# Kernel optimization log

Measured on AMD Instinct MI355X. Metric: run time of the kernel, lower is better.

Reference implementation:

```python
import jax, jax.numpy as jnp
import numpy as np

N, DIM = 8192, 128

def setup_inputs() -> dict:
    key = jax.random.key(0)
    ks = jax.random.split(key, 9)
    s = 1.0 / np.sqrt(DIM)
    return {
        "x": jax.random.normal(ks[0], (N, DIM), dtype=jnp.float32),
        "Wq": jax.random.uniform(ks[1], (DIM, DIM), jnp.float32, -s, s),
        "bq": jax.random.uniform(ks[2], (DIM,), jnp.float32, -s, s),
        "Wk": jax.random.uniform(ks[3], (DIM, DIM), jnp.float32, -s, s),
        "bk": jax.random.uniform(ks[4], (DIM,), jnp.float32, -s, s),
        "Wv": jax.random.uniform(ks[5], (DIM, DIM), jnp.float32, -s, s),
        "bv": jax.random.uniform(ks[6], (DIM,), jnp.float32, -s, s),
        "Wo": jax.random.uniform(ks[7], (DIM, DIM), jnp.float32, -s, s),
        "bo": jax.random.uniform(ks[8], (DIM,), jnp.float32, -s, s),
    }

def reference(x, Wq, bq, Wk, bk, Wv, bv, Wo, bo):
    # nn.Linear: y = x @ W.T + b
    Q = x @ Wq.T + bq                      # [N, d]
    K = x @ Wk.T + bk                      # [N, d]
    V = x @ Wv.T + bv                      # [N, d]
    scale = 1.0 / jnp.sqrt(jnp.asarray(x.shape[-1], x.dtype))
    scores = (Q @ K.T) * scale             # [N, N] — matches original O(n^2) math
    attn = jax.nn.softmax(scores, axis=-1)
    out = attn @ V                         # [N, d]
    return out @ Wo.T + bo
```

## Files before the change

### kernel.cpp

```cpp
#include <hip/hip_runtime.h>
#include <math.h>


typedef __bf16 bf16x8 __attribute__((ext_vector_type(8)));
typedef float f32x4 __attribute__((ext_vector_type(4)));
typedef float f32x16 __attribute__((ext_vector_type(16)));
typedef unsigned int u32x4 __attribute__((ext_vector_type(4)));
typedef unsigned int u32x2 __attribute__((ext_vector_type(2)));
typedef unsigned short us16;

#define NTOK 8192
#define CHUNKS 8

static constexpr float SCALE_L2E = 0.08838834764831845f * 1.4426950408889634f;

__device__ __forceinline__ unsigned f2bf_u(float x) {
    unsigned u = __builtin_bit_cast(unsigned, x);
    return (u + 0x7FFFu + ((u >> 16) & 1u)) >> 16;
}

__device__ __forceinline__ unsigned pk_bf16(float x, float y) {
    unsigned a = __builtin_bit_cast(unsigned, x) + 0x8000u;
    unsigned b = __builtin_bit_cast(unsigned, y) + 0x8000u;
#if __has_builtin(__builtin_amdgcn_perm)
    return __builtin_amdgcn_perm(b, a, 0x07060302u);
#else
    return (a >> 16) | (b & 0xFFFF0000u);
#endif
}

__device__ __forceinline__ unsigned cvtpk_bf16(float x, float y) {
    unsigned r;
    asm("v_cvt_pk_bf16_f32 %0, %1, %2" : "=v"(r) : "v"(x), "v"(y));
    return r;
}

__device__ __forceinline__ void plswap(unsigned& a, unsigned& b) {
    asm("v_permlane32_swap_b32 %0, %1" : "+v"(a), "+v"(b));
}

__device__ __forceinline__ void pl16swap(unsigned& a, unsigned& b) {
    asm("v_permlane16_swap_b32 %0, %1" : "+v"(a), "+v"(b));
}

__device__ __forceinline__ float fexp2(float x) {
#if __has_builtin(__builtin_amdgcn_exp2f)
    return __builtin_amdgcn_exp2f(x);
#else
    return exp2f(x);
#endif
}

__device__ __forceinline__ bf16x8 ld_frag(const us16* p) {
    u32x4 u = *reinterpret_cast<const u32x4*>(p);
    return __builtin_bit_cast(bf16x8, u);
}

__device__ __forceinline__ bf16x8 cvt_frag(const float* p) {
    f32x4 a = *reinterpret_cast<const f32x4*>(p);
    f32x4 b = *reinterpret_cast<const f32x4*>(p + 4);
    u32x4 o;
    o[0] = f2bf_u(a[0]) | (f2bf_u(a[1]) << 16);
    o[1] = f2bf_u(a[2]) | (f2bf_u(a[3]) << 16);
    o[2] = f2bf_u(b[0]) | (f2bf_u(b[1]) << 16);
    o[3] = f2bf_u(b[2]) | (f2bf_u(b[3]) << 16);
    return __builtin_bit_cast(bf16x8, o);
}

__global__ __launch_bounds__(256) void proj_qkv(
    const float* __restrict__ x,
    const float* __restrict__ wq, const float* __restrict__ bq,
    const float* __restrict__ wk, const float* __restrict__ bk,
    const float* __restrict__ wv, const float* __restrict__ bv,
    us16* __restrict__ Qb, us16* __restrict__ Kb, us16* __restrict__ Vt)
{
    __shared__ us16 ldsT[4][16 * 136];

    int z = blockIdx.x >> 7;
    int tile = blockIdx.x & 127;
    const float* W = z == 0 ? wq : z == 1 ? wk : wv;
    const float* bias = z == 0 ? bq : z == 1 ? bk : bv;
    float osc = z == 0 ? SCALE_L2E : 1.0f;

    int w = threadIdx.x >> 6, lane = threadIdx.x & 63;
    int quad = lane >> 4, l15 = lane & 15;
    int rbase = tile * 64 + w * 16;

    bf16x8 af[4];
#pragma unroll
    for (int ks = 0; ks < 4; ++ks)
        af[ks] = cvt_frag(x + (rbase + l15) * 128 + ks * 32 + quad * 8);

    f32x4 acc[8];
#pragma unroll
    for (int nt = 0; nt < 8; ++nt) acc[nt] = f32x4{0.f, 0.f, 0.f, 0.f};

#pragma unroll
    for (int nt = 0; nt < 8; ++nt) {
#pragma unroll
        for (int ks = 0; ks < 4; ++ks) {
            bf16x8 bf = cvt_frag(W + (nt * 16 + l15) * 128 + ks * 32 + quad * 8);
            acc[nt] = __builtin_amdgcn_mfma_f32_16x16x32_bf16(af[ks], bf, acc[nt], 0, 0, 0);
        }
    }

    if (z < 2) {
        us16* T = &ldsT[w][0];
        us16* Out = z == 0 ? Qb : Kb;
#pragma unroll
        for (int nt = 0; nt < 8; ++nt) {
            float bb = bias[nt * 16 + l15];
#pragma unroll
            for (int r = 0; r < 4; ++r)
                T[(quad * 4 + r) * 136 + nt * 16 + l15] =
                    (us16)f2bf_u((acc[nt][r] + bb) * osc);
        }
        asm volatile("s_waitcnt lgkmcnt(0)" ::: "memory");
        __builtin_amdgcn_sched_barrier(0);
        int row = lane >> 2, seg = lane & 3;
        const us16* src = T + row * 136 + seg * 32;
        us16* dst = Out + (rbase + row) * 128 + seg * 32;
#pragma unroll
        for (int c = 0; c < 4; ++c)
            *reinterpret_cast<u32x4*>(dst + c * 8) =
                *reinterpret_cast<const u32x4*>(src + c * 8);
    } else {
#pragma unroll
        for (int nt = 0; nt < 8; ++nt) {
            float bb = bias[nt * 16 + l15];
            int d = nt * 16 + l15, r0 = rbase + quad * 4;
            u32x2 pk;
            pk[0] = f2bf_u(acc[nt][0] + bb) | (f2bf_u(acc[nt][1] + bb) << 16);
            pk[1] = f2bf_u(acc[nt][2] + bb) | (f2bf_u(acc[nt][3] + bb) << 16);
            *reinterpret_cast<u32x2*>(Vt + d * NTOK + r0) = pk;
        }
    }
}

__global__ __launch_bounds__(256, 2) void attn(
    const us16* __restrict__ Qb, const us16* __restrict__ Kb,
    const us16* __restrict__ Vt,
    float* __restrict__ Opart, float* __restrict__ Lpart)
{
    __shared__ us16 ldsK[64 * 136];
    __shared__ us16 ldsV[128 * 72];

    int qtile = blockIdx.x >> 3, chunk = blockIdx.x & 7;
    int tid = threadIdx.x, w = tid >> 6, lane = tid & 63;
    int quad = lane >> 4, l15 = lane & 15;
    int qb0 = qtile * 128 + w * 32;

    bf16x8 qf[2][4];
#pragma unroll
    for (int mt = 0; mt < 2; ++mt)
#pragma unroll
        for (int ks = 0; ks < 4; ++ks)
            qf[mt][ks] = ld_frag(Qb + (qb0 + mt * 16 + l15) * 128 + ks * 32 + quad * 8);

    f32x4 o[2][8];
#pragma unroll
    for (int mt = 0; mt < 2; ++mt)
#pragma unroll
        for (int dt = 0; dt < 8; ++dt) o[mt][dt] = f32x4{0.f, 0.f, 0.f, 0.f};

    f32x4 lacc[2];
    lacc[0] = f32x4{0.f, 0.f, 0.f, 0.f};
    lacc[1] = f32x4{0.f, 0.f, 0.f, 0.f};

    u32x4 onesu;
    onesu[0] = onesu[1] = onesu[2] = onesu[3] = 0x3F803F80u;
    bf16x8 ones = __builtin_bit_cast(bf16x8, onesu);

    for (int it = 0; it < 16; ++it) {
        int kk = chunk * 1024 + it * 64;
#pragma unroll
        for (int c = 0; c < 4; ++c) {
            int idx = tid + c * 256;
            int r = idx >> 4, cc = idx & 15;
            *reinterpret_cast<u32x4*>(ldsK + r * 136 + cc * 8) =
                *reinterpret_cast<const u32x4*>(Kb + (kk + r) * 128 + cc * 8);
        }
#pragma unroll
        for (int c = 0; c < 4; ++c) {
            int idx = tid + c * 256;
            int r = idx >> 3, cc = idx & 7;
            *reinterpret_cast<u32x4*>(ldsV + r * 72 + cc * 8) =
                *reinterpret_cast<const u32x4*>(Vt + r * NTOK + kk + cc * 8);
        }
        __syncthreads();

        f32x4 s[2][4];
#pragma unroll
        for (int mt = 0; mt < 2; ++mt)
#pragma unroll
            for (int nt = 0; nt < 4; ++nt) s[mt][nt] = f32x4{0.f, 0.f, 0.f, 0.f};

        __builtin_amdgcn_s_setprio(1);
#pragma unroll
        for (int nt = 0; nt < 4; ++nt) {
#pragma unroll
            for (int ks = 0; ks < 4; ++ks) {
                bf16x8 kf = ld_frag(ldsK + (nt * 16 + l15) * 136 + ks * 32 + quad * 8);
                s[0][nt] = __builtin_amdgcn_mfma_f32_16x16x32_bf16(kf, qf[0][ks], s[0][nt], 0, 0, 0);
                s[1][nt] = __builtin_amdgcn_mfma_f32_16x16x32_bf16(kf, qf[1][ks], s[1][nt], 0, 0, 0);
            }
        }
        __builtin_amdgcn_s_setprio(0);

        bf16x8 afP[2][2];
#pragma unroll
        for (int mt = 0; mt < 2; ++mt) {
            unsigned W[4][2];
#pragma unroll
            for (int nt = 0; nt < 4; ++nt) {
                float p0 = fexp2(s[mt][nt][0]);
                float p1 = fexp2(s[mt][nt][1]);
                float p2 = fexp2(s[mt][nt][2]);
                float p3 = fexp2(s[mt][nt][3]);
                W[nt][0] = cvtpk_bf16(p0, p1);
                W[nt][1] = cvtpk_bf16(p2, p3);
            }
#pragma unroll
            for (int k2 = 0; k2 < 2; ++k2) {
                u32x4 f;
                {
                    unsigned X = W[2 * k2][0], Y = W[2 * k2 + 1][0];
                    plswap(X, Y); pl16swap(X, Y);
                    f[0] = X; f[2] = Y;
                }
                {
                    unsigned X = W[2 * k2][1], Y = W[2 * k2 + 1][1];
                    plswap(X, Y); pl16swap(X, Y);
                    f[1] = X; f[3] = Y;
                }
                afP[mt][k2] = __builtin_bit_cast(bf16x8, f);
            }
        }

        lacc[0] = __builtin_amdgcn_mfma_f32_16x16x32_bf16(afP[0][0], ones, lacc[0], 0, 0, 0);
        lacc[0] = __builtin_amdgcn_mfma_f32_16x16x32_bf16(afP[0][1], ones, lacc[0], 0, 0, 0);
        lacc[1] = __builtin_amdgcn_mfma_f32_16x16x32_bf16(afP[1][0], ones, lacc[1], 0, 0, 0);
        lacc[1] = __builtin_amdgcn_mfma_f32_16x16x32_bf16(afP[1][1], ones, lacc[1], 0, 0, 0);

        __builtin_amdgcn_s_setprio(1);
#pragma unroll
        for (int dt = 0; dt < 8; ++dt) {
#pragma unroll
            for (int k2 = 0; k2 < 2; ++k2) {
                bf16x8 bv = ld_frag(ldsV + (dt * 16 + l15) * 72 + k2 * 32 + quad * 8);
                o[0][dt] = __builtin_amdgcn_mfma_f32_16x16x32_bf16(afP[0][k2], bv, o[0][dt], 0, 0, 0);
                o[1][dt] = __builtin_amdgcn_mfma_f32_16x16x32_bf16(afP[1][k2], bv, o[1][dt], 0, 0, 0);
            }
        }
        __builtin_amdgcn_s_setprio(0);
        __syncthreads();
    }

#pragma unroll
    for (int mt = 0; mt < 2; ++mt)
#pragma unroll
        for (int dt = 0; dt < 8; ++dt)
#pragma unroll
            for (int r = 0; r < 4; ++r) {
                int row = qb0 + mt * 16 + quad * 4 + r;
                Opart[(size_t)(chunk * NTOK + row) * 128 + dt * 16 + l15] = o[mt][dt][r];
            }
    if (l15 == 0) {
#pragma unroll
        for (int mt = 0; mt < 2; ++mt)
#pragma unroll
            for (int r = 0; r < 4; ++r) {
                int row = qb0 + mt * 16 + quad * 4 + r;
                Lpart[chunk * NTOK + row] = lacc[mt][r];
            }
    }
}

__global__ __launch_bounds__(256) void combine_proj(
    const float* __restrict__ Opart, const float* __restrict__ Lpart,
    const float* __restrict__ Wo, const float* __restrict__ bo,
    float* __restrict__ out)
{
    __shared__ us16 ldsO[32 * 136];
    __shared__ float ldsL[32];

    int tile = blockIdx.x, t = threadIdx.x;
    int r0 = tile * 32;

    if (t < 32) {
        float L = 0.f;
#pragma unroll
        for (int c = 0; c < CHUNKS; ++c) L += Lpart[c * NTOK + r0 + t];
        ldsL[t] = 1.0f / L;
    }

    f32x4 acc[4];
#pragma unroll
    for (int j = 0; j < 4; ++j) acc[j] = f32x4{0.f, 0.f, 0.f, 0.f};

#pragma unroll
    for (int c = 0; c < CHUNKS; ++c) {
        const float* src = Opart + (size_t)(c * NTOK + r0) * 128;
#pragma unroll
        for (int j = 0; j < 4; ++j) {
            f32x4 v = *reinterpret_cast<const f32x4*>(src + j * 1024 + t * 4);
            acc[j] += v;
        }
    }
    __syncthreads();

#pragma unroll
    for (int j = 0; j < 4; ++j) {
        int flat = j * 1024 + t * 4;
        int row = flat >> 7, col = flat & 127;
        float sc = ldsL[row];
        u32x2 wv;
        wv[0] = pk_bf16(acc[j][0] * sc, acc[j][1] * sc);
        wv[1] = pk_bf16(acc[j][2] * sc, acc[j][3] * sc);
        *reinterpret_cast<u32x2*>(ldsO + row * 136 + col) = wv;
    }
    __syncthreads();

    int w = t >> 6, lane = t & 63;
    int l31 = lane & 31, hi = lane >> 5;

    bf16x8 af[8];
#pragma unroll
    for (int ks = 0; ks < 8; ++ks)
        af[ks] = ld_frag(ldsO + l31 * 136 + ks * 16 + hi * 8);

    f32x16 acc2;
#pragma unroll
    for (int r = 0; r < 16; ++r) acc2[r] = 0.f;

#pragma unroll
    for (int ks = 0; ks < 8; ++ks) {
        bf16x8 bfw = cvt_frag(Wo + (w * 32 + l31) * 128 + ks * 16 + hi * 8);
        acc2 = __builtin_amdgcn_mfma_f32_32x32x16_bf16(af[ks], bfw, acc2, 0, 0, 0);
    }

    float bb = bo[w * 32 + l31];
#pragma unroll
    for (int r = 0; r < 16; ++r) {
        int m = (r & 3) + 8 * (r >> 2) + 4 * hi;
        out[(size_t)(r0 + m) * 128 + w * 32 + l31] = acc2[r] + bb;
    }
}

extern "C" void kernel_launch(void* const* d_in, const int* in_sizes, int n_in,
                              void* d_out, int out_size, void* d_ws, size_t ws_size,
                              hipStream_t stream)
{
    const float* x  = (const float*)d_in[0];
    const float* Wq = (const float*)d_in[1];
    const float* bq = (const float*)d_in[2];
    const float* Wk = (const float*)d_in[3];
    const float* bk = (const float*)d_in[4];
    const float* Wv = (const float*)d_in[5];
    const float* bv = (const float*)d_in[6];
    const float* Wo = (const float*)d_in[7];
    const float* bo = (const float*)d_in[8];

    char* ws = (char*)d_ws;
    const size_t MB = 1024 * 1024;
    us16* Qb  = (us16*)(ws + 0 * MB);
    us16* Kb  = (us16*)(ws + 2 * MB);
    us16* Vt  = (us16*)(ws + 4 * MB);
    float* Lp = (float*)(ws + 6 * MB);
    float* Op = (float*)(ws + 7 * MB);

    proj_qkv<<<384, 256, 0, stream>>>(x, Wq, bq, Wk, bk, Wv, bv, Qb, Kb, Vt);
    attn<<<512, 256, 0, stream>>>(Qb, Kb, Vt, Op, Lp);
    combine_proj<<<256, 256, 0, stream>>>(Op, Lp, Wo, bo, (float*)d_out);
}
```

Baseline: 141.7 us.

## Double-buffer K/V tiles in LDS with register prefetch of next tile

Adds a second LDS buffer for K and V tiles. The next tile's global loads are issued into registers before the current tile's MFMA work, and written to the alternate LDS buffer afterwards, which removes one barrier per iteration. This aims to hide global memory latency behind compute. In exchange it doubles LDS use (about 70KB per block, which may limit two blocks per CU) and adds 32 VGPRs of staging data, raising register pressure under launch_bounds(256,2).

```diff
diff --git a/kernel.cpp b/kernel.cpp
--- a/kernel.cpp
+++ b/kernel.cpp
@@ -142,13 +142,14 @@
     const us16* __restrict__ Vt,
     float* __restrict__ Opart, float* __restrict__ Lpart)
 {
-    __shared__ us16 ldsK[64 * 136];
-    __shared__ us16 ldsV[128 * 72];
+    __shared__ us16 ldsK[2][64 * 136];
+    __shared__ us16 ldsV[2][128 * 72];
 
     int qtile = blockIdx.x >> 3, chunk = blockIdx.x & 7;
     int tid = threadIdx.x, w = tid >> 6, lane = tid & 63;
     int quad = lane >> 4, l15 = lane & 15;
     int qb0 = qtile * 128 + w * 32;
+    int k0 = chunk * 1024;
 
     bf16x8 qf[2][4];
 #pragma unroll
@@ -171,23 +172,40 @@
     onesu[0] = onesu[1] = onesu[2] = onesu[3] = 0x3F803F80u;
     bf16x8 ones = __builtin_bit_cast(bf16x8, onesu);
 
+#pragma unroll
+    for (int c = 0; c < 4; ++c) {
+        int idx = tid + c * 256, r = idx >> 4, cc = idx & 15;
+        *reinterpret_cast<u32x4*>(&ldsK[0][0] + r * 136 + cc * 8) =
+            *reinterpret_cast<const u32x4*>(Kb + (k0 + r) * 128 + cc * 8);
+    }
+#pragma unroll
+    for (int c = 0; c < 4; ++c) {
+        int idx = tid + c * 256, r = idx >> 3, cc = idx & 7;
+        *reinterpret_cast<u32x4*>(&ldsV[0][0] + r * 72 + cc * 8) =
+            *reinterpret_cast<const u32x4*>(Vt + (size_t)r * NTOK + k0 + cc * 8);
+    }
+    __syncthreads();
+
     for (int it = 0; it < 16; ++it) {
-        int kk = chunk * 1024 + it * 64;
-#pragma unroll
-        for (int c = 0; c < 4; ++c) {
-            int idx = tid + c * 256;
-            int r = idx >> 4, cc = idx & 15;
-            *reinterpret_cast<u32x4*>(ldsK + r * 136 + cc * 8) =
-                *reinterpret_cast<const u32x4*>(Kb + (kk + r) * 128 + cc * 8);
-        }
-#pragma unroll
-        for (int c = 0; c < 4; ++c) {
-            int idx = tid + c * 256;
-            int r = idx >> 3, cc = idx & 7;
-            *reinterpret_cast<u32x4*>(ldsV + r * 72 + cc * 8) =
-                *reinterpret_cast<const u32x4*>(Vt + r * NTOK + kk + cc * 8);
-        }
-        __syncthreads();
+        int cur = it & 1;
+        const us16* K_ = &ldsK[cur][0];
+        const us16* V_ = &ldsV[cur][0];
+
+        u32x4 kreg[4], vreg[4];
+        if (it < 15) {
+            int kk = k0 + (it + 1) * 64;
+#pragma unroll
+            for (int c = 0; c < 4; ++c) {
+                int idx = tid + c * 256, r = idx >> 4, cc = idx & 15;
+                kreg[c] = *reinterpret_cast<const u32x4*>(Kb + (kk + r) * 128 + cc * 8);
+            }
+#pragma unroll
+            for (int c = 0; c < 4; ++c) {
+                int idx = tid + c * 256, r = idx >> 3, cc = idx & 7;
+                vreg[c] = *reinterpret_cast<const u32x4*>(Vt + (size_t)r * NTOK + kk + cc * 8);
+            }
+            __builtin_amdgcn_sched_barrier(0);
+        }
 
         f32x4 s[2][4];
 #pragma unroll
@@ -200,7 +218,7 @@
         for (int nt = 0; nt < 4; ++nt) {
 #pragma unroll
             for (int ks = 0; ks < 4; ++ks) {
-                bf16x8 kf = ld_frag(ldsK + (nt * 16 + l15) * 136 + ks * 32 + quad * 8);
+                bf16x8 kf = ld_frag(K_ + (nt * 16 + l15) * 136 + ks * 32 + quad * 8);
                 s[0][nt] = __builtin_amdgcn_mfma_f32_16x16x32_bf16(kf, qf[0][ks], s[0][nt], 0, 0, 0);
                 s[1][nt] = __builtin_amdgcn_mfma_f32_16x16x32_bf16(kf, qf[1][ks], s[1][nt], 0, 0, 0);
             }
@@ -247,12 +265,26 @@
         for (int dt = 0; dt < 8; ++dt) {
 #pragma unroll
             for (int k2 = 0; k2 < 2; ++k2) {
-                bf16x8 bv = ld_frag(ldsV + (dt * 16 + l15) * 72 + k2 * 32 + quad * 8);
+                bf16x8 bv = ld_frag(V_ + (dt * 16 + l15) * 72 + k2 * 32 + quad * 8);
                 o[0][dt] = __builtin_amdgcn_mfma_f32_16x16x32_bf16(afP[0][k2], bv, o[0][dt], 0, 0, 0);
                 o[1][dt] = __builtin_amdgcn_mfma_f32_16x16x32_bf16(afP[1][k2], bv, o[1][dt], 0, 0, 0);
             }
         }
         __builtin_amdgcn_s_setprio(0);
+
+        if (it < 15) {
+            __builtin_amdgcn_sched_barrier(0);
+#pragma unroll
+            for (int c = 0; c < 4; ++c) {
+                int idx = tid + c * 256, r = idx >> 4, cc = idx & 15;
+                *reinterpret_cast<u32x4*>(&ldsK[cur ^ 1][0] + r * 136 + cc * 8) = kreg[c];
+            }
+#pragma unroll
+            for (int c = 0; c < 4; ++c) {
+                int idx = tid + c * 256, r = idx >> 3, cc = idx & 7;
+                *reinterpret_cast<u32x4*>(&ldsV[cur ^ 1][0] + r * 72 + cc * 8) = vreg[c];
+            }
+        }
         __syncthreads();
     }
 
```

New measurement: 139.6 us. Within noise of the previous version (-1.5%).
